# Optimization experiments

Hardware: AMD Instinct MI355X
Metric: run time of the kernel (lower is better)

Reference implementation:

```python
import jax, jax.numpy as jnp
import numpy as np

HIDDEN = 1280
HEADS = 16
HEAD_DIM = HIDDEN // HEADS  # 80
B, N = 2, 2048


def _rotate_half(x):
    half = x.shape[-1] // 2
    return jnp.concatenate([-x[..., half:], x[..., :half]], axis=-1)


def setup_inputs() -> dict:
    key = jax.random.key(0)
    ks = jax.random.split(key, 7)
    x = jax.random.normal(ks[0], (B, N, HIDDEN), dtype=jnp.float32)
    cos = jax.random.uniform(ks[1], (N, HEAD_DIM), dtype=jnp.float32)
    sin = jax.random.uniform(ks[2], (N, HEAD_DIM), dtype=jnp.float32)
    s = 1.0 / np.sqrt(HIDDEN)
    qkv_w = jax.random.normal(ks[3], (HIDDEN, 3 * HIDDEN), dtype=jnp.float32) * s
    qkv_b = jax.random.normal(ks[4], (3 * HIDDEN,), dtype=jnp.float32) * 0.02
    proj_w = jax.random.normal(ks[5], (HIDDEN, HIDDEN), dtype=jnp.float32) * s
    proj_b = jax.random.normal(ks[6], (HIDDEN,), dtype=jnp.float32) * 0.02
    return {"x": x, "cos": cos, "sin": sin, "qkv_w": qkv_w, "qkv_b": qkv_b,
            "proj_w": proj_w, "proj_b": proj_b}


def reference(x, cos, sin, qkv_w, qkv_b, proj_w, proj_b):
    b, n, _ = x.shape
    scale = 1.0 / np.sqrt(HEAD_DIM).astype(np.float32)
    # fused QKV projection
    qkv = x @ qkv_w + qkv_b                                # [b, n, 3*hidden]
    qkv = qkv.reshape(b, n, 3, HEADS, HEAD_DIM)
    qkv = jnp.transpose(qkv, (2, 0, 3, 1, 4))              # [3, b, h, n, hd]
    q, k, v = qkv[0], qkv[1], qkv[2]
    # 2D RoPE
    cos_b = cos[None, None, :, :]
    sin_b = sin[None, None, :, :]
    q = q * cos_b + _rotate_half(q) * sin_b
    k = k * cos_b + _rotate_half(k) * sin_b
    # manual softmax attention
    scores = jnp.einsum('bhqd,bhkd->bhqk', q, k) * scale   # [b, h, n, n]
    attn = jax.nn.softmax(scores, axis=-1)
    out = jnp.einsum('bhqk,bhkd->bhqd', attn, v)           # [b, h, n, hd]
    out = jnp.transpose(out, (0, 2, 1, 3)).reshape(b, n, HIDDEN)
    return out @ proj_w + proj_b
```

## Files before the change

### kernel.cpp

```cpp
#include <hip/hip_runtime.h>
#include <hip/hip_bf16.h>
#include <math.h>

#define HIDDEN 1280
#define HEADS 16
#define HD 80
#define HALF 40
#define BB 2
#define NN 2048
#define MROWS (BB * NN)
#define QSCALE ((float)(0.11180339887498949 * 1.4426950408889634))

typedef __attribute__((ext_vector_type(8))) _Float16 f16x8;
typedef __attribute__((ext_vector_type(4))) float f32x4;

#define AS1 __attribute__((address_space(1)))
#define AS3 __attribute__((address_space(3)))

__device__ __forceinline__ void splitf16(float x, ushort& hi, ushort& lo) {
    _Float16 h = (_Float16)x;
    _Float16 l = (_Float16)(x - (float)h);
    hi = __builtin_bit_cast(ushort, h);
    lo = __builtin_bit_cast(ushort, l);
}

__device__ __forceinline__ ushort f2h(float x) {
    _Float16 h = (_Float16)x;
    return __builtin_bit_cast(ushort, h);
}

__global__ __launch_bounds__(256) void split_f16_kernel(
    const float* __restrict__ in, ushort* __restrict__ hi,
    ushort* __restrict__ lo, int n4)
{
    int i = blockIdx.x * 256 + threadIdx.x;
    if (i >= n4) return;
    float4 v = ((const float4*)in)[i];
    ushort4 h, l;
    splitf16(v.x, h.x, l.x);
    splitf16(v.y, h.y, l.y);
    splitf16(v.z, h.z, l.z);
    splitf16(v.w, h.w, l.w);
    ((ushort4*)hi)[i] = h;
    ((ushort4*)lo)[i] = l;
}

__global__ __launch_bounds__(256) void tsplit_f16_kernel(
    const float* __restrict__ W, ushort* __restrict__ T, int K, int N)
{
    __shared__ float s[32][33];
    const int n0 = blockIdx.x * 32;
    const int k0 = blockIdx.y * 32;
    {
        int tn = threadIdx.x & 31, tk = threadIdx.x >> 5;
        #pragma unroll
        for (int i = 0; i < 4; ++i)
            s[tk + i * 8][tn] = W[(size_t)(k0 + tk + i * 8) * N + n0 + tn];
    }
    __syncthreads();
    {
        int tk = threadIdx.x & 31, tn = threadIdx.x >> 5;
        #pragma unroll
        for (int i = 0; i < 4; ++i)
            T[(size_t)(n0 + tn + i * 8) * K + k0 + tk] = f2h(s[tk][tn + i * 8]);
    }
}

#define BM 128
#define BN 128
#define BK 32

__global__ __launch_bounds__(256) void gemm_f16x2_kernel(
    const ushort* __restrict__ Ahi, const ushort* __restrict__ Alo,
    const ushort* __restrict__ Bh,
    const float* __restrict__ bias, float* __restrict__ C,
    int M, int N, int K)
{
    __shared__ __align__(16) ushort lds[3 * 128 * 32];

    const int tid = threadIdx.x;
    const int wid = tid >> 6;
    const int lane = tid & 63;
    const int col0 = blockIdx.x * BN;
    const int row0 = blockIdx.y * BM;
    const int wy = wid >> 1, wx = wid & 1;
    const int lrow = lane >> 2;
    const int lchunk = lane & 3;

    f32x4 acc[4][4] = {};

    for (int k0 = 0; k0 < K; k0 += BK) {
        __syncthreads();
        #pragma unroll
        for (int i = 0; i < 6; ++i) {
            int s = wid + i * 4;
            int tile = s >> 3, t = s & 7;
            const ushort* src = (tile == 0) ? Ahi : (tile == 1) ? Alo : Bh;
            int srow = (tile < 2) ? row0 : col0;
            const ushort* g = src + (size_t)(srow + t * 16 + lrow) * K + k0 + lchunk * 8;
            ushort* l = lds + tile * 4096 + t * 512 + lane * 8;
            __builtin_amdgcn_global_load_lds(
                (const AS1 unsigned int*)g, (AS3 unsigned int*)l, 16, 0, 0);
        }
        __syncthreads();

        const int q = lane >> 4;
        const int r = lane & 15;
        f16x8 ah[4], al[4], bf[4];
        #pragma unroll
        for (int i = 0; i < 4; ++i) {
            int arow = wy * 64 + i * 16 + r;
            ah[i] = *(const f16x8*)(lds + 0 * 4096 + arow * 32 + q * 8);
            al[i] = *(const f16x8*)(lds + 1 * 4096 + arow * 32 + q * 8);
            int brow = wx * 64 + i * 16 + r;
            bf[i] = *(const f16x8*)(lds + 2 * 4096 + brow * 32 + q * 8);
        }
        #pragma unroll
        for (int i = 0; i < 4; ++i) {
            #pragma unroll
            for (int j = 0; j < 4; ++j) {
                acc[i][j] = __builtin_amdgcn_mfma_f32_16x16x32_f16(al[i], bf[j], acc[i][j], 0, 0, 0);
                acc[i][j] = __builtin_amdgcn_mfma_f32_16x16x32_f16(ah[i], bf[j], acc[i][j], 0, 0, 0);
            }
        }
    }

    const int q = lane >> 4, r = lane & 15;
    #pragma unroll
    for (int i = 0; i < 4; ++i) {
        #pragma unroll
        for (int j = 0; j < 4; ++j) {
            int col = col0 + wx * 64 + j * 16 + r;
            float b = bias[col];
            #pragma unroll
            for (int v = 0; v < 4; ++v) {
                int row = row0 + wy * 64 + i * 16 + q * 4 + v;
                C[(size_t)row * N + col] = acc[i][j][v] + b;
            }
        }
    }
}

__global__ __launch_bounds__(512, 2) void gemm_f16x2_256_kernel(
    const ushort* __restrict__ Ahi, const ushort* __restrict__ Alo,
    const ushort* __restrict__ Bh,
    const float* __restrict__ bias, float* __restrict__ C,
    int M, int N, int K, int nbx)
{
    __shared__ __align__(16) ushort lds[3 * 3 * 8192];

    const int tid = threadIdx.x;
    const int wid = tid >> 6;
    const int lane = tid & 63;
    const int q = lane >> 4, r = lane & 15;
    const int wr = wid >> 2, wc = wid & 3;

    int id = blockIdx.x;
    {
        int nwg = gridDim.x;
        if ((nwg & 7) == 0) {
            int c = nwg >> 3;
            id = (id & 7) * c + (id >> 3);
        }
    }
    const int row0 = (id / nbx) * 256;
    const int col0 = (id % nbx) * 256;

    const ushort* gsrc[6];
    int ldst[6];
    #pragma unroll
    for (int j = 0; j < 6; ++j) {
        int pj = j >> 1;
        int rloc = wid * 32 + (j & 1) * 16 + (lane >> 2);
        int sl = (lane & 3) ^ ((rloc >> 1) & 3);
        const ushort* base = (pj == 0) ? Ahi : (pj == 1) ? Alo : Bh;
        int grow = ((pj < 2) ? row0 : col0) + rloc;
        gsrc[j] = base + (size_t)grow * K + sl * 8;
        ldst[j] = pj * 8192 + (wid * 32 + (j & 1) * 16) * 32 + lane * 8;
    }

    const int NT = K / 32;

    #pragma unroll
    for (int j = 0; j < 6; ++j)
        __builtin_amdgcn_global_load_lds((const AS1 unsigned int*)(gsrc[j]),
            (AS3 unsigned int*)(lds + ldst[j]), 16, 0, 0);
    #pragma unroll
    for (int j = 0; j < 6; ++j)
        __builtin_amdgcn_global_load_lds((const AS1 unsigned int*)(gsrc[j] + 32),
            (AS3 unsigned int*)(lds + 24576 + ldst[j]), 16, 0, 0);
    asm volatile("s_waitcnt vmcnt(6)" ::: "memory");
    __builtin_amdgcn_s_barrier();

    const int soff = (q ^ ((r >> 1) & 3)) * 8;
    const int arow0 = wr * 128 + r;
    const int brow0 = wc * 64 + r;

    f32x4 acc[8][4] = {};
    f16x8 ah[4], al[4], bf[4];

    int cb = 0;
    int nb = 49152;

    for (int t = 0; t < NT; ++t) {
        const ushort* A0 = lds + cb;
        const ushort* A1 = lds + cb + 8192;
        const ushort* Bp = lds + cb + 16384;
        ushort* nbuf = lds + nb;
        const bool st = (t + 2 < NT);
        const int ko = (t + 2) * 32;

        #pragma unroll
        for (int m = 0; m < 4; ++m) {
            int ro = (arow0 + m * 16) * 32 + soff;
            ah[m] = *(const f16x8*)(A0 + ro);
            al[m] = *(const f16x8*)(A1 + ro);
        }
        #pragma unroll
        for (int n = 0; n < 2; ++n)
            bf[n] = *(const f16x8*)(Bp + (brow0 + n * 16) * 32 + soff);
        if (st) {
            __builtin_amdgcn_global_load_lds((const AS1 unsigned int*)(gsrc[0] + ko),
                (AS3 unsigned int*)(nbuf + ldst[0]), 16, 0, 0);
            __builtin_amdgcn_global_load_lds((const AS1 unsigned int*)(gsrc[1] + ko),
                (AS3 unsigned int*)(nbuf + ldst[1]), 16, 0, 0);
        }
        __builtin_amdgcn_s_barrier();
        asm volatile("s_waitcnt lgkmcnt(0)" ::: "memory");
        __builtin_amdgcn_sched_barrier(0);
        __builtin_amdgcn_s_setprio(1);
        #pragma unroll
        for (int m = 0; m < 4; ++m) {
            #pragma unroll
            for (int n = 0; n < 2; ++n) {
                acc[m][n] = __builtin_amdgcn_mfma_f32_16x16x32_f16(al[m], bf[n], acc[m][n], 0, 0, 0);
                acc[m][n] = __builtin_amdgcn_mfma_f32_16x16x32_f16(ah[m], bf[n], acc[m][n], 0, 0, 0);
            }
        }
        __builtin_amdgcn_s_setprio(0);
        __builtin_amdgcn_s_barrier();

        #pragma unroll
        for (int n = 2; n < 4; ++n)
            bf[n] = *(const f16x8*)(Bp + (brow0 + n * 16) * 32 + soff);
        if (st) {
            __builtin_amdgcn_global_load_lds((const AS1 unsigned int*)(gsrc[2] + ko),
                (AS3 unsigned int*)(nbuf + ldst[2]), 16, 0, 0);
            __builtin_amdgcn_global_load_lds((const AS1 unsigned int*)(gsrc[3] + ko),
                (AS3 unsigned int*)(nbuf + ldst[3]), 16, 0, 0);
        }
        __builtin_amdgcn_s_barrier();
        asm volatile("s_waitcnt lgkmcnt(0)" ::: "memory");
        __builtin_amdgcn_sched_barrier(0);
        __builtin_amdgcn_s_setprio(1);
        #pragma unroll
        for (int m = 0; m < 4; ++m) {
            #pragma unroll
            for (int n = 2; n < 4; ++n) {
                acc[m][n] = __builtin_amdgcn_mfma_f32_16x16x32_f16(al[m], bf[n], acc[m][n], 0, 0, 0);
                acc[m][n] = __builtin_amdgcn_mfma_f32_16x16x32_f16(ah[m], bf[n], acc[m][n], 0, 0, 0);
            }
        }
        __builtin_amdgcn_s_setprio(0);
        __builtin_amdgcn_s_barrier();

        #pragma unroll
        for (int m = 0; m < 4; ++m) {
            int ro = (arow0 + (m + 4) * 16) * 32 + soff;
            ah[m] = *(const f16x8*)(A0 + ro);
            al[m] = *(const f16x8*)(A1 + ro);
        }
        if (st) {
            __builtin_amdgcn_global_load_lds((const AS1 unsigned int*)(gsrc[4] + ko),
                (AS3 unsigned int*)(nbuf + ldst[4]), 16, 0, 0);
            __builtin_amdgcn_global_load_lds((const AS1 unsigned int*)(gsrc[5] + ko),
                (AS3 unsigned int*)(nbuf + ldst[5]), 16, 0, 0);
        }
        __builtin_amdgcn_s_barrier();
        asm volatile("s_waitcnt lgkmcnt(0)" ::: "memory");
        __builtin_amdgcn_sched_barrier(0);
        __builtin_amdgcn_s_setprio(1);
        #pragma unroll
        for (int m = 0; m < 4; ++m) {
            #pragma unroll
            for (int n = 2; n < 4; ++n) {
                acc[m + 4][n] = __builtin_amdgcn_mfma_f32_16x16x32_f16(al[m], bf[n], acc[m + 4][n], 0, 0, 0);
                acc[m + 4][n] = __builtin_amdgcn_mfma_f32_16x16x32_f16(ah[m], bf[n], acc[m + 4][n], 0, 0, 0);
            }
        }
        __builtin_amdgcn_s_setprio(0);
        __builtin_amdgcn_s_barrier();

        __builtin_amdgcn_s_setprio(1);
        #pragma unroll
        for (int m = 0; m < 4; ++m) {
            #pragma unroll
            for (int n = 0; n < 2; ++n) {
                acc[m + 4][n] = __builtin_amdgcn_mfma_f32_16x16x32_f16(al[m], bf[n], acc[m + 4][n], 0, 0, 0);
                acc[m + 4][n] = __builtin_amdgcn_mfma_f32_16x16x32_f16(ah[m], bf[n], acc[m + 4][n], 0, 0, 0);
            }
        }
        __builtin_amdgcn_s_setprio(0);
        if (st)
            asm volatile("s_waitcnt vmcnt(6)" ::: "memory");
        else if (t + 1 < NT)
            asm volatile("s_waitcnt vmcnt(0)" ::: "memory");
        __builtin_amdgcn_s_barrier();

        cb += 24576; if (cb == 73728) cb = 0;
        nb += 24576; if (nb == 73728) nb = 0;
    }

    #pragma unroll
    for (int m = 0; m < 8; ++m) {
        #pragma unroll
        for (int n = 0; n < 4; ++n) {
            int col = col0 + wc * 64 + n * 16 + r;
            float b = bias[col];
            #pragma unroll
            for (int v = 0; v < 4; ++v) {
                int row = row0 + wr * 128 + m * 16 + q * 4 + v;
                C[(size_t)row * N + col] = acc[m][n][v] + b;
            }
        }
    }
}

__global__ __launch_bounds__(256) void rope_split_kernel(
    const float* __restrict__ qkv, const float* __restrict__ cos_t,
    const float* __restrict__ sin_t,
    ushort* __restrict__ qf, ushort* __restrict__ kf,
    ushort* __restrict__ vt)
{
    __shared__ float s_v[64][84];
    const int tid = threadIdx.x;
    const int b = blockIdx.z, h = blockIdx.y;
    const int n0 = blockIdx.x * 64;
    const int bh = b * HEADS + h;

    #pragma unroll
    for (int i = 0; i < 5; ++i) {
        int u = tid + i * 256;
        int n = u / 20, c = u % 20;
        const float* src = qkv + (size_t)(b * NN + n0 + n) * 3840 + 2 * HIDDEN + h * HD + c * 4;
        *(float4*)(&s_v[n][c * 4]) = *(const float4*)src;
    }

    for (int u = tid; u < 640; u += 256) {
        int n = u / 10, p = u % 10;
        int d = p * 4;
        int ng = n0 + n;
        size_t rowb = (size_t)(b * NN + ng) * 3840;
        float4 c0 = *(const float4*)(cos_t + ng * HD + d);
        float4 c1 = *(const float4*)(cos_t + ng * HD + d + HALF);
        float4 s0 = *(const float4*)(sin_t + ng * HD + d);
        float4 s1 = *(const float4*)(sin_t + ng * HD + d + HALF);
        size_t qo = ((size_t)bh * NN + ng) * 96;
        {
            float4 x0 = *(const float4*)(qkv + rowb + h * HD + d);
            float4 x1 = *(const float4*)(qkv + rowb + h * HD + d + HALF);
            ushort4 h4a, h4b;
            h4a.x = f2h((x0.x * c0.x - x1.x * s0.x) * QSCALE);
            h4a.y = f2h((x0.y * c0.y - x1.y * s0.y) * QSCALE);
            h4a.z = f2h((x0.z * c0.z - x1.z * s0.z) * QSCALE);
            h4a.w = f2h((x0.w * c0.w - x1.w * s0.w) * QSCALE);
            h4b.x = f2h((x1.x * c1.x + x0.x * s1.x) * QSCALE);
            h4b.y = f2h((x1.y * c1.y + x0.y * s1.y) * QSCALE);
            h4b.z = f2h((x1.z * c1.z + x0.z * s1.z) * QSCALE);
            h4b.w = f2h((x1.w * c1.w + x0.w * s1.w) * QSCALE);
            *(ushort4*)(qf + qo + d) = h4a;
            *(ushort4*)(qf + qo + d + HALF) = h4b;
        }
        {
            float4 x0 = *(const float4*)(qkv + rowb + HIDDEN + h * HD + d);
            float4 x1 = *(const float4*)(qkv + rowb + HIDDEN + h * HD + d + HALF);
            ushort4 h4a, h4b;
            h4a.x = f2h(x0.x * c0.x - x1.x * s0.x);
            h4a.y = f2h(x0.y * c0.y - x1.y * s0.y);
            h4a.z = f2h(x0.z * c0.z - x1.z * s0.z);
            h4a.w = f2h(x0.w * c0.w - x1.w * s0.w);
            h4b.x = f2h(x1.x * c1.x + x0.x * s1.x);
            h4b.y = f2h(x1.y * c1.y + x0.y * s1.y);
            h4b.z = f2h(x1.z * c1.z + x0.z * s1.z);
            h4b.w = f2h(x1.w * c1.w + x0.w * s1.w);
            *(ushort4*)(kf + qo + d) = h4a;
            *(ushort4*)(kf + qo + d + HALF) = h4b;
        }
    }

    {
        int which = tid >> 7;
        int u = tid & 127;
        int n = u >> 1, part = u & 1;
        size_t o = ((size_t)bh * NN + n0 + n) * 96 + 80 + part * 8;
        uint4 z = {0u, 0u, 0u, 0u};
        if (which == 0) *(uint4*)(qf + o) = z;
        else            *(uint4*)(kf + o) = z;
    }
    __syncthreads();

    for (int u = tid; u < 320; u += 256) {
        int d = u >> 2, nc = u & 3;
        ushort hs[16];
        #pragma unroll
        for (int kk = 0; kk < 16; ++kk)
            hs[kk] = f2h(s_v[nc * 16 + kk][d]);
        size_t o = ((size_t)bh * HD + d) * NN + n0 + nc * 16;
        uint4 w0, w1;
        w0.x = (uint)hs[0] | ((uint)hs[1] << 16);
        w0.y = (uint)hs[2] | ((uint)hs[3] << 16);
        w0.z = (uint)hs[4] | ((uint)hs[5] << 16);
        w0.w = (uint)hs[6] | ((uint)hs[7] << 16);
        w1.x = (uint)hs[8] | ((uint)hs[9] << 16);
        w1.y = (uint)hs[10] | ((uint)hs[11] << 16);
        w1.z = (uint)hs[12] | ((uint)hs[13] << 16);
        w1.w = (uint)hs[14] | ((uint)hs[15] << 16);
        *(uint4*)(vt + o) = w0;
        *(uint4*)(vt + o + 8) = w1;
    }
}

__global__ __launch_bounds__(512, 4) void attn_mfma_kernel(
    const ushort* __restrict__ qf, const ushort* __restrict__ kf,
    const ushort* __restrict__ vt,
    ushort* __restrict__ ao_hi, ushort* __restrict__ ao_lo)
{
    __shared__ __align__(16) ushort lds[34816];
    _Float16* p_s = (_Float16*)(lds + 26624);

    const int tid = threadIdx.x;
    const int wave = tid >> 6, lane = tid & 63;
    const int quad = lane >> 4, r = lane & 15;
    const int b = blockIdx.z, h = blockIdx.y;
    const int bh = b * HEADS + h;
    const int q0 = blockIdx.x * 128;

    const size_t kb = (size_t)bh * NN * 96;
    const size_t vb = (size_t)bh * HD * NN;

    const ushort* gptr[4];
    int ldso[4];
    #pragma unroll
    for (int i = 0; i < 4; ++i) {
        int s = wave + i * 8;
        if (s < 16) {
            int row = s * 4 + (lane >> 4);
            int t = lane & 15;
            int g = t ^ (row & 7);
            if (g >= 12) g = 0;
            gptr[i] = kf + kb + (size_t)row * 96 + g * 8;
            ldso[i] = s * 512 + lane * 8;
        } else if (s < 26) {
            int ts = s - 16;
            gptr[i] = vt + vb + (size_t)(ts * 8 + (lane >> 3)) * NN
                      + (size_t)(((lane & 7) ^ (lane >> 3)) * 8);
            ldso[i] = 8192 + ts * 512 + lane * 8;
        } else {
            gptr[i] = nullptr;
            ldso[i] = 0;
        }
    }

    f16x8 qfr[3];
    #pragma unroll
    for (int c = 0; c < 3; ++c) {
        size_t o = ((size_t)bh * NN + q0 + wave * 16 + r) * 96 + c * 32 + quad * 8;
        qfr[c] = *(const f16x8*)(qf + o);
    }

    f32x4 oacc[5] = {};
    float l_part[4] = {};

    #pragma unroll
    for (int i = 0; i < 4; ++i) {
        int s = wave + i * 8;
        if (s < 26) {
            __builtin_amdgcn_global_load_lds((const AS1 unsigned int*)gptr[i],
                (AS3 unsigned int*)(lds + ldso[i]), 16, 0, 0);
            gptr[i] += (s < 16) ? 6144 : 64;
        }
    }
    asm volatile("s_waitcnt vmcnt(0)" ::: "memory");
    __builtin_amdgcn_s_barrier();

    int cur = 0;
    for (int j0 = 0; j0 < NN; j0 += 64) {
        const int nxt = 13312 - cur;
        if (j0 + 64 < NN) {
            #pragma unroll
            for (int i = 0; i < 4; ++i) {
                int s = wave + i * 8;
                if (s < 26) {
                    __builtin_amdgcn_global_load_lds((const AS1 unsigned int*)gptr[i],
                        (AS3 unsigned int*)(lds + nxt + ldso[i]), 16, 0, 0);
                    gptr[i] += (s < 16) ? 6144 : 64;
                }
            }
        }

        const ushort* k_s = lds + cur;
        const _Float16* v_s = (const _Float16*)(lds + cur + 8192);

        f32x4 sc[4] = {};
        __builtin_amdgcn_s_setprio(1);
        #pragma unroll
        for (int jt = 0; jt < 4; ++jt) {
            f16x8 kbf[3];
            int j = jt * 16 + r;
            #pragma unroll
            for (int c = 0; c < 3; ++c) {
                int ch = (c * 4 + quad) ^ (r & 7);
                kbf[c] = *(const f16x8*)(k_s + j * 128 + ch * 8);
            }
            #pragma unroll
            for (int c = 0; c < 3; ++c)
                sc[jt] = __builtin_amdgcn_mfma_f32_16x16x32_f16(qfr[c], kbf[c], sc[jt], 0, 0, 0);
        }
        __builtin_amdgcn_s_setprio(0);

        #pragma unroll
        for (int v = 0; v < 4; ++v) {
            float ps = 0.0f;
            #pragma unroll
            for (int jt = 0; jt < 4; ++jt) {
                float p = __builtin_amdgcn_exp2f(sc[jt][v]);
                sc[jt][v] = p;
                ps += p;
            }
            l_part[v] += ps;
        }
        {
            int rowbase = wave * 16 + quad * 4;
            #pragma unroll
            for (int jt = 0; jt < 4; ++jt) {
                int bks = (jt * 2 + (r >> 3)) ^ (quad << 1);
                #pragma unroll
                for (int v = 0; v < 4; ++v)
                    p_s[(rowbase + v) * 64 + bks * 8 + (r & 7)] = (_Float16)sc[jt][v];
            }
        }

        f16x8 pa[2];
        #pragma unroll
        for (int cc = 0; cc < 2; ++cc) {
            int rowp = wave * 16 + r;
            int bks = (cc * 4 + quad) ^ (((r >> 2) & 3) << 1);
            pa[cc] = *(const f16x8*)(p_s + rowp * 64 + bks * 8);
        }

        __builtin_amdgcn_s_setprio(1);
        #pragma unroll
        for (int dt = 0; dt < 5; ++dt)
            #pragma unroll
            for (int cc = 0; cc < 2; ++cc) {
                int ck = (cc * 4 + quad) ^ (r & 7);
                f16x8 vbf = *(const f16x8*)(v_s + (dt * 16 + r) * 64 + ck * 8);
                oacc[dt] = __builtin_amdgcn_mfma_f32_16x16x32_f16(pa[cc], vbf, oacc[dt], 0, 0, 0);
            }
        __builtin_amdgcn_s_setprio(0);

        asm volatile("s_waitcnt vmcnt(0)" ::: "memory");
        __builtin_amdgcn_s_barrier();
        cur = nxt;
    }

    float inv_l[4];
    #pragma unroll
    for (int v = 0; v < 4; ++v) {
        float l = l_part[v];
        l += __shfl_xor(l, 1);
        l += __shfl_xor(l, 2);
        l += __shfl_xor(l, 4);
        l += __shfl_xor(l, 8);
        inv_l[v] = 1.0f / l;
    }

    __syncthreads();
    #pragma unroll
    for (int v = 0; v < 4; ++v) {
        int row = wave * 16 + quad * 4 + v;
        #pragma unroll
        for (int dt = 0; dt < 5; ++dt) {
            float o = oacc[dt][v] * inv_l[v];
            ushort hh, ll;
            splitf16(o, hh, ll);
            lds[row * 80 + dt * 16 + r] = hh;
            lds[10240 + row * 80 + dt * 16 + r] = ll;
        }
    }
    __syncthreads();
    {
        size_t gbase = ((size_t)b * NN + q0) * HIDDEN + h * HD;
        #pragma unroll
        for (int i = 0; i < 5; ++i) {
            int u = tid + i * 512;
            int plane = u / 1280, idx = u % 1280;
            int row = idx / 10, part = idx % 10;
            uint4 w = *(const uint4*)(lds + plane * 10240 + idx * 8);
            ushort* dst = (plane ? ao_lo : ao_hi) + gbase + (size_t)row * HIDDEN + part * 8;
            *(uint4*)dst = w;
        }
    }
}

extern "C" void kernel_launch(void* const* d_in, const int* in_sizes, int n_in,
                              void* d_out, int out_size, void* d_ws, size_t ws_size,
                              hipStream_t stream)
{
    const float* x      = (const float*)d_in[0];
    const float* cos_t  = (const float*)d_in[1];
    const float* sin_t  = (const float*)d_in[2];
    const float* qkv_w  = (const float*)d_in[3];
    const float* qkv_b  = (const float*)d_in[4];
    const float* proj_w = (const float*)d_in[5];
    const float* proj_b = (const float*)d_in[6];
    float* out = (float*)d_out;

    char* ws = (char*)d_ws;
    float*  qkv   = (float*)ws;
    ushort* ao_hi = (ushort*)ws;
    ushort* ao_lo = (ushort*)(ws + 10485760);
    ushort* wT    = (ushort*)(ws + 62914560);
    ushort* vt    = (ushort*)(ws + 62914560);
    ushort* a_hi  = (ushort*)(ws + 82575360);
    ushort* a_lo  = (ushort*)(ws + 93061120);
    ushort* q_f   = (ushort*)(ws + 83886080);
    ushort* k_f   = (ushort*)(ws + 96468992);

    split_f16_kernel<<<(MROWS * HIDDEN / 4 + 255) / 256, 256, 0, stream>>>(
        x, a_hi, a_lo, MROWS * HIDDEN / 4);

    tsplit_f16_kernel<<<dim3(3 * HIDDEN / 32, HIDDEN / 32), 256, 0, stream>>>(
        qkv_w, wT, HIDDEN, 3 * HIDDEN);

    gemm_f16x2_256_kernel<<<dim3((MROWS / 256) * (3 * HIDDEN / 256)), 512, 0, stream>>>(
        a_hi, a_lo, wT, qkv_b, qkv, MROWS, 3 * HIDDEN, HIDDEN, 3 * HIDDEN / 256);

    rope_split_kernel<<<dim3(NN / 64, HEADS, BB), 256, 0, stream>>>(
        qkv, cos_t, sin_t, q_f, k_f, vt);

    attn_mfma_kernel<<<dim3(NN / 128, HEADS, BB), 512, 0, stream>>>(
        q_f, k_f, vt, ao_hi, ao_lo);

    tsplit_f16_kernel<<<dim3(HIDDEN / 32, HIDDEN / 32), 256, 0, stream>>>(
        proj_w, wT, HIDDEN, HIDDEN);

    gemm_f16x2_kernel<<<dim3(HIDDEN / BN, MROWS / BM), 256, 0, stream>>>(
        ao_hi, ao_lo, wT, proj_b, out, MROWS, HIDDEN, HIDDEN);
}
```

Baseline: 318.1 us.

## Shrink QKV GEMM tile to 256x128 with double buffering and higher occupancy

```diff
diff --git a/kernel.cpp b/kernel.cpp
--- a/kernel.cpp
+++ b/kernel.cpp
@@ -141,19 +141,20 @@
     }
 }
 
-__global__ __launch_bounds__(512, 2) void gemm_f16x2_256_kernel(
+__global__ __launch_bounds__(512, 4) void gemm_f16x2_256x128_kernel(
     const ushort* __restrict__ Ahi, const ushort* __restrict__ Alo,
     const ushort* __restrict__ Bh,
     const float* __restrict__ bias, float* __restrict__ C,
     int M, int N, int K, int nbx)
 {
-    __shared__ __align__(16) ushort lds[3 * 3 * 8192];
+    __shared__ __align__(16) ushort lds[2 * 20480];
 
     const int tid = threadIdx.x;
     const int wid = tid >> 6;
     const int lane = tid & 63;
     const int q = lane >> 4, r = lane & 15;
-    const int wr = wid >> 2, wc = wid & 3;
+    const int wr = wid >> 1;
+    const int wc = wid & 1;
 
     int id = blockIdx.x;
     {
@@ -164,51 +165,51 @@
         }
     }
     const int row0 = (id / nbx) * 256;
-    const int col0 = (id % nbx) * 256;
-
-    const ushort* gsrc[6];
-    int ldst[6];
-    #pragma unroll
-    for (int j = 0; j < 6; ++j) {
-        int pj = j >> 1;
-        int rloc = wid * 32 + (j & 1) * 16 + (lane >> 2);
-        int sl = (lane & 3) ^ ((rloc >> 1) & 3);
-        const ushort* base = (pj == 0) ? Ahi : (pj == 1) ? Alo : Bh;
-        int grow = ((pj < 2) ? row0 : col0) + rloc;
-        gsrc[j] = base + (size_t)grow * K + sl * 8;
-        ldst[j] = pj * 8192 + (wid * 32 + (j & 1) * 16) * 32 + lane * 8;
+    const int col0 = (id % nbx) * 128;
+
+    const ushort* gsrc[5];
+    int ldst[5];
+    #pragma unroll
+    for (int j = 0; j < 5; ++j) {
+        if (j < 4) {
+            int p = j >> 1;
+            int rloc = wid * 32 + (j & 1) * 16 + (lane >> 2);
+            int sl = (lane & 3) ^ ((rloc >> 1) & 3);
+            const ushort* base = p ? Alo : Ahi;
+            gsrc[j] = base + (size_t)(row0 + rloc) * K + sl * 8;
+            ldst[j] = p * 8192 + (wid * 32 + (j & 1) * 16) * 32 + lane * 8;
+        } else {
+            int rloc = wid * 16 + (lane >> 2);
+            int sl = (lane & 3) ^ ((rloc >> 1) & 3);
+            gsrc[4] = Bh + (size_t)(col0 + rloc) * K + sl * 8;
+            ldst[4] = 16384 + wid * 512 + lane * 8;
+        }
     }
 
     const int NT = K / 32;
 
     #pragma unroll
-    for (int j = 0; j < 6; ++j)
+    for (int j = 0; j < 5; ++j)
         __builtin_amdgcn_global_load_lds((const AS1 unsigned int*)(gsrc[j]),
             (AS3 unsigned int*)(lds + ldst[j]), 16, 0, 0);
-    #pragma unroll
-    for (int j = 0; j < 6; ++j)
-        __builtin_amdgcn_global_load_lds((const AS1 unsigned int*)(gsrc[j] + 32),
-            (AS3 unsigned int*)(lds + 24576 + ldst[j]), 16, 0, 0);
-    asm volatile("s_waitcnt vmcnt(6)" ::: "memory");
+    asm volatile("s_waitcnt vmcnt(0)" ::: "memory");
     __builtin_amdgcn_s_barrier();
 
     const int soff = (q ^ ((r >> 1) & 3)) * 8;
-    const int arow0 = wr * 128 + r;
+    const int arow0 = wr * 64 + r;
     const int brow0 = wc * 64 + r;
 
-    f32x4 acc[8][4] = {};
-    f16x8 ah[4], al[4], bf[4];
+    f32x4 acc[4][4] = {};
+    f16x8 ah[4], al[4], bf[2];
 
     int cb = 0;
-    int nb = 49152;
-
     for (int t = 0; t < NT; ++t) {
         const ushort* A0 = lds + cb;
         const ushort* A1 = lds + cb + 8192;
         const ushort* Bp = lds + cb + 16384;
-        ushort* nbuf = lds + nb;
-        const bool st = (t + 2 < NT);
-        const int ko = (t + 2) * 32;
+        ushort* nbuf = lds + (20480 - cb);
+        const bool st = (t + 1 < NT);
+        const int ko = (t + 1) * 32;
 
         #pragma unroll
         for (int m = 0; m < 4; ++m) {
@@ -224,6 +225,8 @@
                 (AS3 unsigned int*)(nbuf + ldst[0]), 16, 0, 0);
             __builtin_amdgcn_global_load_lds((const AS1 unsigned int*)(gsrc[1] + ko),
                 (AS3 unsigned int*)(nbuf + ldst[1]), 16, 0, 0);
+            __builtin_amdgcn_global_load_lds((const AS1 unsigned int*)(gsrc[2] + ko),
+                (AS3 unsigned int*)(nbuf + ldst[2]), 16, 0, 0);
         }
         __builtin_amdgcn_s_barrier();
         asm volatile("s_waitcnt lgkmcnt(0)" ::: "memory");
@@ -241,13 +244,13 @@
         __builtin_amdgcn_s_barrier();
 
         #pragma unroll
-        for (int n = 2; n < 4; ++n)
-            bf[n] = *(const f16x8*)(Bp + (brow0 + n * 16) * 32 + soff);
+        for (int n = 0; n < 2; ++n)
+            bf[n] = *(const f16x8*)(Bp + (brow0 + (n + 2) * 16) * 32 + soff);
         if (st) {
-            __builtin_amdgcn_global_load_lds((const AS1 unsigned int*)(gsrc[2] + ko),
-                (AS3 unsigned int*)(nbuf + ldst[2]), 16, 0, 0);
             __builtin_amdgcn_global_load_lds((const AS1 unsigned int*)(gsrc[3] + ko),
                 (AS3 unsigned int*)(nbuf + ldst[3]), 16, 0, 0);
+            __builtin_amdgcn_global_load_lds((const AS1 unsigned int*)(gsrc[4] + ko),
+                (AS3 unsigned int*)(nbuf + ldst[4]), 16, 0, 0);
         }
         __builtin_amdgcn_s_barrier();
         asm volatile("s_waitcnt lgkmcnt(0)" ::: "memory");
@@ -256,70 +259,26 @@
         #pragma unroll
         for (int m = 0; m < 4; ++m) {
             #pragma unroll
-            for (int n = 2; n < 4; ++n) {
-                acc[m][n] = __builtin_amdgcn_mfma_f32_16x16x32_f16(al[m], bf[n], acc[m][n], 0, 0, 0);
-                acc[m][n] = __builtin_amdgcn_mfma_f32_16x16x32_f16(ah[m], bf[n], acc[m][n], 0, 0, 0);
+            for (int n = 0; n < 2; ++n) {
+                acc[m][n + 2] = __builtin_amdgcn_mfma_f32_16x16x32_f16(al[m], bf[n], acc[m][n + 2], 0, 0, 0);
+                acc[m][n + 2] = __builtin_amdgcn_mfma_f32_16x16x32_f16(ah[m], bf[n], acc[m][n + 2], 0, 0, 0);
             }
         }
         __builtin_amdgcn_s_setprio(0);
+        asm volatile("s_waitcnt vmcnt(0)" ::: "memory");
         __builtin_amdgcn_s_barrier();
-
-        #pragma unroll
-        for (int m = 0; m < 4; ++m) {
-            int ro = (arow0 + (m + 4) * 16) * 32 + soff;
-            ah[m] = *(const f16x8*)(A0 + ro);
-            al[m] = *(const f16x8*)(A1 + ro);
-        }
-        if (st) {
-            __builtin_amdgcn_global_load_lds((const AS1 unsigned int*)(gsrc[4] + ko),
-                (AS3 unsigned int*)(nbuf + ldst[4]), 16, 0, 0);
-            __builtin_amdgcn_global_load_lds((const AS1 unsigned int*)(gsrc[5] + ko),
-                (AS3 unsigned int*)(nbuf + ldst[5]), 16, 0, 0);
-        }
-        __builtin_amdgcn_s_barrier();
-        asm volatile("s_waitcnt lgkmcnt(0)" ::: "memory");
-        __builtin_amdgcn_sched_barrier(0);
-        __builtin_amdgcn_s_setprio(1);
-        #pragma unroll
-        for (int m = 0; m < 4; ++m) {
-            #pragma unroll
-            for (int n = 2; n < 4; ++n) {
-                acc[m + 4][n] = __builtin_amdgcn_mfma_f32_16x16x32_f16(al[m], bf[n], acc[m + 4][n], 0, 0, 0);
-                acc[m + 4][n] = __builtin_amdgcn_mfma_f32_16x16x32_f16(ah[m], bf[n], acc[m + 4][n], 0, 0, 0);
-            }
-        }
-        __builtin_amdgcn_s_setprio(0);
-        __builtin_amdgcn_s_barrier();
-
-        __builtin_amdgcn_s_setprio(1);
-        #pragma unroll
-        for (int m = 0; m < 4; ++m) {
-            #pragma unroll
-            for (int n = 0; n < 2; ++n) {
-                acc[m + 4][n] = __builtin_amdgcn_mfma_f32_16x16x32_f16(al[m], bf[n], acc[m + 4][n], 0, 0, 0);
-                acc[m + 4][n] = __builtin_amdgcn_mfma_f32_16x16x32_f16(ah[m], bf[n], acc[m + 4][n], 0, 0, 0);
-            }
-        }
-        __builtin_amdgcn_s_setprio(0);
-        if (st)
-            asm volatile("s_waitcnt vmcnt(6)" ::: "memory");
-        else if (t + 1 < NT)
-            asm volatile("s_waitcnt vmcnt(0)" ::: "memory");
-        __builtin_amdgcn_s_barrier();
-
-        cb += 24576; if (cb == 73728) cb = 0;
-        nb += 24576; if (nb == 73728) nb = 0;
-    }
-
-    #pragma unroll
-    for (int m = 0; m < 8; ++m) {
+        cb = 20480 - cb;
+    }
+
+    #pragma unroll
+    for (int m = 0; m < 4; ++m) {
         #pragma unroll
         for (int n = 0; n < 4; ++n) {
             int col = col0 + wc * 64 + n * 16 + r;
             float b = bias[col];
             #pragma unroll
             for (int v = 0; v < 4; ++v) {
-                int row = row0 + wr * 128 + m * 16 + q * 4 + v;
+                int row = row0 + wr * 64 + m * 16 + q * 4 + v;
                 C[(size_t)row * N + col] = acc[m][n][v] + b;
             }
         }
@@ -633,8 +592,8 @@
     tsplit_f16_kernel<<<dim3(3 * HIDDEN / 32, HIDDEN / 32), 256, 0, stream>>>(
         qkv_w, wT, HIDDEN, 3 * HIDDEN);
 
-    gemm_f16x2_256_kernel<<<dim3((MROWS / 256) * (3 * HIDDEN / 256)), 512, 0, stream>>>(
-        a_hi, a_lo, wT, qkv_b, qkv, MROWS, 3 * HIDDEN, HIDDEN, 3 * HIDDEN / 256);
+    gemm_f16x2_256x128_kernel<<<dim3((MROWS / 256) * (3 * HIDDEN / 128)), 512, 0, stream>>>(
+        a_hi, a_lo, wT, qkv_b, qkv, MROWS, 3 * HIDDEN, HIDDEN, 3 * HIDDEN / 128);
 
     rope_split_kernel<<<dim3(NN / 64, HEADS, BB), 256, 0, stream>>>(
         qkv, cos_t, sin_t, q_f, k_f, vt);
```

Result: slower. 326.1 us (+2.5%).
